# Kernel tuning notes

Hardware: AMD Instinct MI355X
Metric: run time of the kernel (lower is better)

## Reference

```python
import jax, jax.numpy as jnp
import numpy as np

HEADS = 4
DIM_HEAD = 32
CHUNK = 1024
GROUPS = 8
EPS = 1e-5


def setup_inputs() -> dict:
    key = jax.random.key(0)
    k1, k2, k3 = jax.random.split(key, 3)
    b, dim, h, w = 8, 64, 96, 96
    inner = HEADS * DIM_HEAD  # 128
    x = jax.random.normal(k1, (b, dim, h, w), dtype=jnp.float32)
    W_qkv = jax.random.normal(k2, (3 * inner, dim), dtype=jnp.float32) * (1.0 / np.sqrt(dim))
    W_out = jax.random.normal(k3, (dim, inner), dtype=jnp.float32) * (1.0 / np.sqrt(inner))
    b_out = jnp.zeros((dim,), dtype=jnp.float32)
    gamma = jnp.ones((dim,), dtype=jnp.float32)
    beta = jnp.zeros((dim,), dtype=jnp.float32)
    return {"x": x, "W_qkv": W_qkv, "W_out": W_out, "b_out": b_out,
            "gamma": gamma, "beta": beta}


def reference(x, W_qkv, W_out, b_out, gamma, beta):
    b, c, h, w = x.shape
    n = h * w
    nch = n // CHUNK  # number of full chunks (n chosen divisible by CHUNK)
    d = DIM_HEAD
    BH = b * HEADS

    # 1x1 conv (no bias) == matmul over channel dim
    xf = x.reshape(b, c, n)
    qkv = jnp.einsum('oc,bcn->bon', W_qkv, xf)          # [b, 3*inner, n]
    q, k, v = jnp.split(qkv, 3, axis=1)                  # each [b, inner, n]

    def chunkify(t):
        # [b, inner, n] -> [BH, nch, d, CHUNK]; slicing i:i+CHUNK on last axis
        # equals reshaping n -> (nch, CHUNK) in order.
        return t.reshape(BH, d, nch, CHUNK).transpose(0, 2, 1, 3)

    qc, kc, vc = chunkify(q), chunkify(k), chunkify(v)

    qs = jax.nn.softmax(qc, axis=-1)  # softmax over chunk spatial positions
    ks = jax.nn.softmax(kc, axis=-2)  # softmax over head channels

    # context = k_chunk^T @ v_chunk : [BH, nch, CHUNK, CHUNK]
    ctx = jnp.einsum('gkdi,gkdj->gkij', ks, vc)
    # chunk_out = q_chunk @ context : [BH, nch, d, CHUNK]
    out = jnp.einsum('gkdi,gkij->gkdj', qs, ctx)

    # concat chunks back along spatial dim, reshape to image layout
    out = out.transpose(0, 2, 1, 3).reshape(b, HEADS * d, h, w)

    # to_out: 1x1 conv with bias, then GroupNorm(8, dim)
    y = jnp.einsum('oc,bchw->bohw', W_out, out) + b_out[None, :, None, None]

    yg = y.reshape(b, GROUPS, c // GROUPS, h, w)
    mu = jnp.mean(yg, axis=(2, 3, 4), keepdims=True)
    var = jnp.var(yg, axis=(2, 3, 4), keepdims=True)
    yn = ((yg - mu) * jax.lax.rsqrt(var + EPS)).reshape(b, c, h, w)
    return yn * gamma[None, :, None, None] + beta[None, :, None, None]
```

## Files before the change

### kernel.cpp

```cpp
#include <hip/hip_runtime.h>
#include <hip/hip_bf16.h>

#define N_POS 9216
#define NCHUNK 9
#define BATCH 8
#define CDIM 64
#define HEADS 4
#define EPS 1e-5f

#define PPART_SZ ((size_t)32 * NCHUNK * 1024)
#define NPART 8
#define UBF_BYTES ((size_t)BATCH * NCHUNK * 64 * 128 * 2)

typedef __attribute__((ext_vector_type(8))) short short8;
typedef __attribute__((ext_vector_type(4))) float f32x4;

static __device__ inline unsigned pk2(float a, float b) {
    __hip_bfloat162 h2(__float2bfloat16(a), __float2bfloat16(b));
    return *reinterpret_cast<unsigned*>(&h2);
}
static __device__ inline float bf2f(short s) {
    union { unsigned u; float f; } c; c.u = ((unsigned)(unsigned short)s) << 16; return c.f;
}

__global__ __launch_bounds__(256) void wprep_kernel(const float* __restrict__ Wqkv,
        __hip_bfloat16* __restrict__ wbf, float* __restrict__ stats) {
    int i = blockIdx.x * 256 + threadIdx.x;
    if (i < 6144) {
        float4 v = ((const float4*)Wqkv)[i];
        uint2 u; u.x = pk2(v.x, v.y); u.y = pk2(v.z, v.w);
        ((uint2*)wbf)[i] = u;
    }
    if (i < 128) stats[i] = 0.f;
}

__global__ __launch_bounds__(256) void qkp_kernel(const float* __restrict__ x,
        const __hip_bfloat16* __restrict__ wbf, float* __restrict__ Pparts) {
    int bx = blockIdx.x;
    int b  = blockIdx.y;
    int ck = bx >> 3, pt = bx & 7;
    __shared__ __align__(16) char lraw[36864];
    __hip_bfloat16 (*xs)[72]  = (__hip_bfloat16(*)[72])lraw;
    __hip_bfloat16 (*skT)[72] = (__hip_bfloat16(*)[72])lraw;
    int t = threadIdx.x, w = t >> 6, l = t & 63;
    int l15 = l & 15, quad = l >> 4;

    f32x4 pac[2][2];
    pac[0][0] = (f32x4){0,0,0,0}; pac[0][1] = (f32x4){0,0,0,0};
    pac[1][0] = (f32x4){0,0,0,0}; pac[1][1] = (f32x4){0,0,0,0};

    for (int half = 0; half < 2; ++half) {
        int n0 = bx * 128 + half * 64;

        {
            int p = t & 63, cbase = (t >> 6) * 16;
            const float* xb = x + (size_t)b * CDIM * N_POS + n0 + p;
            #pragma unroll
            for (int j = 0; j < 16; j += 4) {
                float v0 = xb[(size_t)(cbase + j + 0) * N_POS];
                float v1 = xb[(size_t)(cbase + j + 1) * N_POS];
                float v2 = xb[(size_t)(cbase + j + 2) * N_POS];
                float v3 = xb[(size_t)(cbase + j + 3) * N_POS];
                uint2 u; u.x = pk2(v0, v1); u.y = pk2(v2, v3);
                *reinterpret_cast<uint2*>(&xs[p][cbase + j]) = u;
            }
        }
        __syncthreads();

        f32x4 acc[4][4];
        #pragma unroll
        for (int mt = 0; mt < 4; ++mt)
            #pragma unroll
            for (int nt = 0; nt < 4; ++nt) acc[mt][nt] = (f32x4){0.f, 0.f, 0.f, 0.f};
        #pragma unroll
        for (int ks = 0; ks < 2; ++ks) {
            int k0 = ks * 32 + quad * 8;
            short8 av[4];
            #pragma unroll
            for (int mt = 0; mt < 4; ++mt)
                av[mt] = *reinterpret_cast<const short8*>(&xs[mt * 16 + l15][k0]);
            #pragma unroll
            for (int nt = 0; nt < 4; ++nt) {
                short8 bw = *reinterpret_cast<const short8*>(wbf + (size_t)(w * 64 + nt * 16 + l15) * 64 + k0);
                #pragma unroll
                for (int mt = 0; mt < 4; ++mt)
                    acc[mt][nt] = __builtin_amdgcn_mfma_f32_16x16x32_bf16(av[mt], bw, acc[mt][nt], 0, 0, 0);
            }
        }
        __syncthreads();

        #pragma unroll
        for (int nt = 0; nt < 4; ++nt) {
            int ch = w * 64 + nt * 16 + l15;
            #pragma unroll
            for (int mt = 0; mt < 4; ++mt) {
                uint2 u;
                u.x = pk2(acc[mt][nt][0], acc[mt][nt][1]);
                u.y = pk2(acc[mt][nt][2], acc[mt][nt][3]);
                *reinterpret_cast<uint2*>(&skT[ch][mt * 16 + quad * 4]) = u;
            }
        }
        __syncthreads();

        {
            int p = t & 63, h = t >> 6;
            float kr[32]; float mx = -1e30f;
            #pragma unroll
            for (int d = 0; d < 32; ++d) { kr[d] = bf2f(*(const short*)&skT[128 + h * 32 + d][p]); mx = fmaxf(mx, kr[d]); }
            float s = 0.f;
            #pragma unroll
            for (int d = 0; d < 32; ++d) { kr[d] = __expf(kr[d] - mx); s += kr[d]; }
            float is = 1.f / s;
            #pragma unroll
            for (int d = 0; d < 32; ++d) skT[128 + h * 32 + d][p] = __float2bfloat16(kr[d] * is);
            #pragma unroll
            for (int d = 0; d < 32; ++d) {
                float qv = bf2f(*(const short*)&skT[h * 32 + d][p]);
                skT[h * 32 + d][p] = __float2bfloat16(__expf(qv));
            }
        }
        __syncthreads();

        #pragma unroll
        for (int step = 0; step < 2; ++step) {
            int k0 = step * 32 + quad * 8;
            short8 bk[2];
            #pragma unroll
            for (int nt = 0; nt < 2; ++nt)
                bk[nt] = *reinterpret_cast<const short8*>(&skT[128 + w * 32 + nt * 16 + l15][k0]);
            #pragma unroll
            for (int mt = 0; mt < 2; ++mt) {
                short8 aq = *reinterpret_cast<const short8*>(&skT[w * 32 + mt * 16 + l15][k0]);
                pac[mt][0] = __builtin_amdgcn_mfma_f32_16x16x32_bf16(aq, bk[0], pac[mt][0], 0, 0, 0);
                pac[mt][1] = __builtin_amdgcn_mfma_f32_16x16x32_bf16(aq, bk[1], pac[mt][1], 0, 0, 0);
            }
        }
        __syncthreads();
    }

    float* Pp = Pparts + (size_t)pt * PPART_SZ + ((size_t)(b * 4 + w) * NCHUNK + ck) * 1024;
    #pragma unroll
    for (int mt = 0; mt < 2; ++mt)
        #pragma unroll
        for (int nt = 0; nt < 2; ++nt)
            #pragma unroll
            for (int r = 0; r < 4; ++r)
                Pp[(mt * 16 + quad * 4 + r) * 32 + nt * 16 + l15] = pac[mt][nt][r];
}

__global__ __launch_bounds__(256) void umat_kernel(const float* __restrict__ Wout,
        const float* __restrict__ Pparts, __hip_bfloat16* __restrict__ Ubf) {
    int ck = blockIdx.x, b = blockIdx.y, h = blockIdx.z;
    int bh = b * 4 + h;
    int t = threadIdx.x;
    __shared__ float Pl[32][32];
    __shared__ float iZ[32];
    size_t base4 = ((size_t)bh * NCHUNK + ck) * 256;
    {
        const float4* P0 = (const float4*)Pparts + base4 + t;
        float4 s = (float4){0.f, 0.f, 0.f, 0.f};
        #pragma unroll
        for (int j = 0; j < NPART; ++j) {
            float4 a = P0[j * (PPART_SZ / 4)];
            s.x += a.x; s.y += a.y; s.z += a.z; s.w += a.w;
        }
        ((float4*)Pl)[t] = s;
    }
    __syncthreads();
    if (t < 32) {
        float s = 0.f;
        #pragma unroll
        for (int c = 0; c < 32; ++c) s += Pl[t][c];
        iZ[t] = 1.f / s;
    }
    __syncthreads();
    int o = t & 63, wv = t >> 6;
    float wz[32];
    {
        const float4* wr = (const float4*)(Wout + (size_t)o * 128 + h * 32);
        #pragma unroll
        for (int j = 0; j < 8; ++j) {
            float4 f = wr[j];
            wz[j*4+0] = f.x * iZ[j*4+0]; wz[j*4+1] = f.y * iZ[j*4+1];
            wz[j*4+2] = f.z * iZ[j*4+2]; wz[j*4+3] = f.w * iZ[j*4+3];
        }
    }
    float ua[8];
    #pragma unroll
    for (int j = 0; j < 8; ++j) ua[j] = 0.f;
    for (int d = 0; d < 32; ++d) {
        float wd = wz[d];
        #pragma unroll
        for (int j = 0; j < 8; ++j) ua[j] += wd * Pl[d][wv * 8 + j];
    }
    uint4 up;
    up.x = pk2(ua[0], ua[1]); up.y = pk2(ua[2], ua[3]);
    up.z = pk2(ua[4], ua[5]); up.w = pk2(ua[6], ua[7]);
    __hip_bfloat16* Up = Ubf + ((size_t)(b * NCHUNK + ck) * 64 + o) * 128 + h * 32 + wv * 8;
    *reinterpret_cast<uint4*>(Up) = up;
}

__global__ __launch_bounds__(256) void vy_kernel(const float* __restrict__ x,
        const __hip_bfloat16* __restrict__ wbf, const __hip_bfloat16* __restrict__ Ubf,
        const float* __restrict__ bout, float* __restrict__ y, float* __restrict__ stats) {
    int bx = blockIdx.x;
    int b  = blockIdx.y;
    int ck = bx >> 3;
    int n0 = bx * 128;
    __shared__ __align__(16) char lraw[34816];
    __hip_bfloat16 (*xs)[72]    = (__hip_bfloat16(*)[72])lraw;
    __hip_bfloat16 (*vbuf)[136] = (__hip_bfloat16(*)[136])lraw;
    __shared__ float gsum[8], gsq[8];
    int t = threadIdx.x, w = t >> 6, l = t & 63;
    int l15 = l & 15, quad = l >> 4;
    if (t < 8) { gsum[t] = 0.f; gsq[t] = 0.f; }

    {
        int p = t & 127, cbase = (t >> 7) * 32;
        const float* xb = x + (size_t)b * CDIM * N_POS + n0 + p;
        #pragma unroll
        for (int j = 0; j < 32; j += 4) {
            float v0 = xb[(size_t)(cbase + j + 0) * N_POS];
            float v1 = xb[(size_t)(cbase + j + 1) * N_POS];
            float v2 = xb[(size_t)(cbase + j + 2) * N_POS];
            float v3 = xb[(size_t)(cbase + j + 3) * N_POS];
            uint2 u; u.x = pk2(v0, v1); u.y = pk2(v2, v3);
            *reinterpret_cast<uint2*>(&xs[p][cbase + j]) = u;
        }
    }
    __syncthreads();

    int nw = w * 32;
    {
        f32x4 vacc[8][2];
        #pragma unroll
        for (int mt = 0; mt < 8; ++mt) { vacc[mt][0] = (f32x4){0,0,0,0}; vacc[mt][1] = (f32x4){0,0,0,0}; }
        #pragma unroll
        for (int ks = 0; ks < 2; ++ks) {
            int k0 = ks * 32 + quad * 8;
            short8 bfr[2];
            #pragma unroll
            for (int nt = 0; nt < 2; ++nt)
                bfr[nt] = *reinterpret_cast<const short8*>(&xs[nw + nt * 16 + l15][k0]);
            #pragma unroll
            for (int mt = 0; mt < 8; ++mt) {
                short8 afr = *reinterpret_cast<const short8*>(wbf + (size_t)(256 + mt * 16 + l15) * 64 + k0);
                vacc[mt][0] = __builtin_amdgcn_mfma_f32_16x16x32_bf16(afr, bfr[0], vacc[mt][0], 0, 0, 0);
                vacc[mt][1] = __builtin_amdgcn_mfma_f32_16x16x32_bf16(afr, bfr[1], vacc[mt][1], 0, 0, 0);
            }
        }
        __syncthreads();

        #pragma unroll
        for (int mt = 0; mt < 8; ++mt)
            #pragma unroll
            for (int nt = 0; nt < 2; ++nt) {
                int p = nw + nt * 16 + l15;
                uint2 u;
                u.x = pk2(vacc[mt][nt][0], vacc[mt][nt][1]);
                u.y = pk2(vacc[mt][nt][2], vacc[mt][nt][3]);
                *reinterpret_cast<uint2*>(&vbuf[p][mt * 16 + quad * 4]) = u;
            }
    }
    __syncthreads();

    const __hip_bfloat16* Ub = Ubf + (size_t)(b * NCHUNK + ck) * 64 * 128;
    f32x4 acc[4][2];
    #pragma unroll
    for (int mt = 0; mt < 4; ++mt) { acc[mt][0] = (f32x4){0,0,0,0}; acc[mt][1] = (f32x4){0,0,0,0}; }
    #pragma unroll
    for (int ks = 0; ks < 4; ++ks) {
        int k0 = ks * 32 + quad * 8;
        short8 bf[2];
        #pragma unroll
        for (int nt = 0; nt < 2; ++nt)
            bf[nt] = *reinterpret_cast<const short8*>(&vbuf[nw + nt * 16 + l15][k0]);
        #pragma unroll
        for (int mt = 0; mt < 4; ++mt) {
            short8 af = *reinterpret_cast<const short8*>(Ub + (size_t)(mt * 16 + l15) * 128 + k0);
            acc[mt][0] = __builtin_amdgcn_mfma_f32_16x16x32_bf16(af, bf[0], acc[mt][0], 0, 0, 0);
            acc[mt][1] = __builtin_amdgcn_mfma_f32_16x16x32_bf16(af, bf[1], acc[mt][1], 0, 0, 0);
        }
    }
    float gsl[4], gql[4];
    #pragma unroll
    for (int mt = 0; mt < 4; ++mt) { gsl[mt] = 0.f; gql[mt] = 0.f; }
    float* yb = y + (size_t)b * CDIM * N_POS;
    int nbase = n0 + nw;
    #pragma unroll
    for (int mt = 0; mt < 4; ++mt) {
        float4 bo = *reinterpret_cast<const float4*>(bout + mt * 16 + quad * 4);
        const float* bop = reinterpret_cast<const float*>(&bo);
        #pragma unroll
        for (int nt = 0; nt < 2; ++nt) {
            int n = nbase + nt * 16 + l15;
            #pragma unroll
            for (int r = 0; r < 4; ++r) {
                int o = mt * 16 + quad * 4 + r;
                float val = acc[mt][nt][r] + bop[r];
                yb[(size_t)o * N_POS + n] = val;
                gsl[mt] += val; gql[mt] += val * val;
            }
        }
    }
    #pragma unroll
    for (int off = 16; off >= 1; off >>= 1) {
        #pragma unroll
        for (int mt = 0; mt < 4; ++mt) {
            gsl[mt] += __shfl_xor(gsl[mt], off, 64);
            gql[mt] += __shfl_xor(gql[mt], off, 64);
        }
    }
    if (l == 0 || l == 32) {
        int qh = quad >> 1;
        #pragma unroll
        for (int mt = 0; mt < 4; ++mt) {
            atomicAdd(&gsum[2 * mt + qh], gsl[mt]);
            atomicAdd(&gsq[2 * mt + qh], gql[mt]);
        }
    }
    __syncthreads();
    if (t < 8) {
        atomicAdd(&stats[(b * 8 + t) * 2],     gsum[t]);
        atomicAdd(&stats[(b * 8 + t) * 2 + 1], gsq[t]);
    }
}

__global__ __launch_bounds__(256) void gn_kernel(float* __restrict__ y,
        const float* __restrict__ stats, const float* __restrict__ gamma,
        const float* __restrict__ beta) {
    int i4 = blockIdx.x * 256 + threadIdx.x;
    if (i4 >= (BATCH * CDIM * N_POS) / 4) return;
    int base = i4 * 4;
    int bc = base / N_POS;
    int c = bc & 63, b = bc >> 6;
    int g = c >> 3;
    float s = stats[(b * 8 + g) * 2], q = stats[(b * 8 + g) * 2 + 1];
    const float invN = 1.f / (8.f * N_POS);
    float mean = s * invN;
    float var = q * invN - mean * mean;
    float sc = rsqrtf(var + EPS);
    float ga = gamma[c] * sc;
    float be = beta[c] - mean * sc * gamma[c];
    float4 v = ((float4*)y)[i4];
    v.x = v.x * ga + be; v.y = v.y * ga + be; v.z = v.z * ga + be; v.w = v.w * ga + be;
    ((float4*)y)[i4] = v;
}

extern "C" void kernel_launch(void* const* d_in, const int* in_sizes, int n_in,
                              void* d_out, int out_size, void* d_ws, size_t ws_size,
                              hipStream_t stream) {
    const float* x     = (const float*)d_in[0];
    const float* Wqkv  = (const float*)d_in[1];
    const float* Wout  = (const float*)d_in[2];
    const float* bout  = (const float*)d_in[3];
    const float* gamma = (const float*)d_in[4];
    const float* beta  = (const float*)d_in[5];
    float* out = (float*)d_out;

    float* stats  = (float*)d_ws;
    float* Pparts = stats + 128;
    __hip_bfloat16* Ubf = (__hip_bfloat16*)(Pparts + NPART * PPART_SZ);
    __hip_bfloat16* wbf = (__hip_bfloat16*)((char*)Ubf + UBF_BYTES);

    wprep_kernel<<<dim3(24), 256, 0, stream>>>(Wqkv, wbf, stats);
    qkp_kernel<<<dim3(72, BATCH), 256, 0, stream>>>(x, wbf, Pparts);
    umat_kernel<<<dim3(NCHUNK, BATCH, HEADS), 256, 0, stream>>>(Wout, Pparts, Ubf);
    vy_kernel<<<dim3(72, BATCH), 256, 0, stream>>>(x, wbf, Ubf, bout, out, stats);
    gn_kernel<<<dim3((BATCH * CDIM * N_POS / 4 + 255) / 256), 256, 0, stream>>>(out, stats, gamma, beta);
}
```

Measured before the change: 125.5 us.

## Fuse GroupNorm into vy kernel via grid-wide barrier, keep y in registers

Removes the separate GroupNorm pass by keeping the to_out accumulators in registers. Every block waits at a global atomic-counter barrier until all 576 blocks have contributed group statistics, then normalizes and writes y once. This avoids writing y, reading it back and rewriting it, roughly 19 MB each way. It relies on all 576 blocks being co-resident (launch bounds of 3 blocks per CU); if they are not, the kernel deadlocks. The barrier also puts a global sync inside the kernel.

```diff
diff --git a/kernel.cpp b/kernel.cpp
--- a/kernel.cpp
+++ b/kernel.cpp
@@ -11,6 +11,7 @@
 #define PPART_SZ ((size_t)32 * NCHUNK * 1024)
 #define NPART 8
 #define UBF_BYTES ((size_t)BATCH * NCHUNK * 64 * 128 * 2)
+#define VY_BLOCKS 576u
 
 typedef __attribute__((ext_vector_type(8))) short short8;
 typedef __attribute__((ext_vector_type(4))) float f32x4;
@@ -31,7 +32,7 @@
         uint2 u; u.x = pk2(v.x, v.y); u.y = pk2(v.z, v.w);
         ((uint2*)wbf)[i] = u;
     }
-    if (i < 128) stats[i] = 0.f;
+    if (i < 256) stats[i] = 0.f;
 }
 
 __global__ __launch_bounds__(256) void qkp_kernel(const float* __restrict__ x,
@@ -51,7 +52,6 @@
 
     for (int half = 0; half < 2; ++half) {
         int n0 = bx * 128 + half * 64;
-
         {
             int p = t & 63, cbase = (t >> 6) * 16;
             const float* xb = x + (size_t)b * CDIM * N_POS + n0 + p;
@@ -200,9 +200,10 @@
     *reinterpret_cast<uint4*>(Up) = up;
 }
 
-__global__ __launch_bounds__(256) void vy_kernel(const float* __restrict__ x,
+__global__ __launch_bounds__(256, 3) void vy_kernel(const float* __restrict__ x,
         const __hip_bfloat16* __restrict__ wbf, const __hip_bfloat16* __restrict__ Ubf,
-        const float* __restrict__ bout, float* __restrict__ y, float* __restrict__ stats) {
+        const float* __restrict__ bout, float* __restrict__ y, float* __restrict__ stats,
+        const float* __restrict__ gamma, const float* __restrict__ beta) {
     int bx = blockIdx.x;
     int b  = blockIdx.y;
     int ck = bx >> 3;
@@ -250,7 +251,6 @@
             }
         }
         __syncthreads();
-
         #pragma unroll
         for (int mt = 0; mt < 8; ++mt)
             #pragma unroll
@@ -285,23 +285,18 @@
     float gsl[4], gql[4];
     #pragma unroll
     for (int mt = 0; mt < 4; ++mt) { gsl[mt] = 0.f; gql[mt] = 0.f; }
-    float* yb = y + (size_t)b * CDIM * N_POS;
-    int nbase = n0 + nw;
     #pragma unroll
     for (int mt = 0; mt < 4; ++mt) {
         float4 bo = *reinterpret_cast<const float4*>(bout + mt * 16 + quad * 4);
         const float* bop = reinterpret_cast<const float*>(&bo);
         #pragma unroll
-        for (int nt = 0; nt < 2; ++nt) {
-            int n = nbase + nt * 16 + l15;
+        for (int nt = 0; nt < 2; ++nt)
             #pragma unroll
             for (int r = 0; r < 4; ++r) {
-                int o = mt * 16 + quad * 4 + r;
                 float val = acc[mt][nt][r] + bop[r];
-                yb[(size_t)o * N_POS + n] = val;
+                acc[mt][nt][r] = val;
                 gsl[mt] += val; gql[mt] += val * val;
             }
-        }
     }
     #pragma unroll
     for (int off = 16; off >= 1; off >>= 1) {
@@ -324,27 +319,43 @@
         atomicAdd(&stats[(b * 8 + t) * 2],     gsum[t]);
         atomicAdd(&stats[(b * 8 + t) * 2 + 1], gsq[t]);
     }
-}
-
-__global__ __launch_bounds__(256) void gn_kernel(float* __restrict__ y,
-        const float* __restrict__ stats, const float* __restrict__ gamma,
-        const float* __restrict__ beta) {
-    int i4 = blockIdx.x * 256 + threadIdx.x;
-    if (i4 >= (BATCH * CDIM * N_POS) / 4) return;
-    int base = i4 * 4;
-    int bc = base / N_POS;
-    int c = bc & 63, b = bc >> 6;
-    int g = c >> 3;
-    float s = stats[(b * 8 + g) * 2], q = stats[(b * 8 + g) * 2 + 1];
+    __threadfence();
+    __syncthreads();
+    if (t == 0) {
+        unsigned* ctr = (unsigned*)(stats + 192);
+        __hip_atomic_fetch_add(ctr, 1u, __ATOMIC_RELEASE, __HIP_MEMORY_SCOPE_AGENT);
+        while (__hip_atomic_load(ctr, __ATOMIC_ACQUIRE, __HIP_MEMORY_SCOPE_AGENT) < VY_BLOCKS)
+            __builtin_amdgcn_s_sleep(8);
+    }
+    __syncthreads();
+
     const float invN = 1.f / (8.f * N_POS);
-    float mean = s * invN;
-    float var = q * invN - mean * mean;
-    float sc = rsqrtf(var + EPS);
-    float ga = gamma[c] * sc;
-    float be = beta[c] - mean * sc * gamma[c];
-    float4 v = ((float4*)y)[i4];
-    v.x = v.x * ga + be; v.y = v.y * ga + be; v.z = v.z * ga + be; v.w = v.w * ga + be;
-    ((float4*)y)[i4] = v;
+    float* yb = y + (size_t)b * CDIM * N_POS;
+    int nbase = n0 + nw;
+    #pragma unroll
+    for (int mt = 0; mt < 4; ++mt) {
+        int g = 2 * mt + (quad >> 1);
+        float s = __hip_atomic_load(&stats[(b * 8 + g) * 2],     __ATOMIC_RELAXED, __HIP_MEMORY_SCOPE_AGENT);
+        float q = __hip_atomic_load(&stats[(b * 8 + g) * 2 + 1], __ATOMIC_RELAXED, __HIP_MEMORY_SCOPE_AGENT);
+        float mean = s * invN;
+        float var = q * invN - mean * mean;
+        float rstd = rsqrtf(var + EPS);
+        float4 ga4 = *reinterpret_cast<const float4*>(gamma + mt * 16 + quad * 4);
+        float4 be4 = *reinterpret_cast<const float4*>(beta + mt * 16 + quad * 4);
+        const float* gap = reinterpret_cast<const float*>(&ga4);
+        const float* bep = reinterpret_cast<const float*>(&be4);
+        #pragma unroll
+        for (int r = 0; r < 4; ++r) {
+            int o = mt * 16 + quad * 4 + r;
+            float sc = gap[r] * rstd;
+            float be = bep[r] - mean * sc;
+            #pragma unroll
+            for (int nt = 0; nt < 2; ++nt) {
+                int n = nbase + nt * 16 + l15;
+                yb[(size_t)o * N_POS + n] = acc[mt][nt][r] * sc + be;
+            }
+        }
+    }
 }
 
 extern "C" void kernel_launch(void* const* d_in, const int* in_sizes, int n_in,
@@ -359,13 +370,12 @@
     float* out = (float*)d_out;
 
     float* stats  = (float*)d_ws;
-    float* Pparts = stats + 128;
+    float* Pparts = stats + 256;
     __hip_bfloat16* Ubf = (__hip_bfloat16*)(Pparts + NPART * PPART_SZ);
     __hip_bfloat16* wbf = (__hip_bfloat16*)((char*)Ubf + UBF_BYTES);
 
     wprep_kernel<<<dim3(24), 256, 0, stream>>>(Wqkv, wbf, stats);
     qkp_kernel<<<dim3(72, BATCH), 256, 0, stream>>>(x, wbf, Pparts);
     umat_kernel<<<dim3(NCHUNK, BATCH, HEADS), 256, 0, stream>>>(Wout, Pparts, Ubf);
-    vy_kernel<<<dim3(72, BATCH), 256, 0, stream>>>(x, wbf, Ubf, bout, out, stats);
-    gn_kernel<<<dim3((BATCH * CDIM * N_POS / 4 + 255) / 256), 256, 0, stream>>>(out, stats, gamma, beta);
-}
+    vy_kernel<<<dim3(72, BATCH), 256, 0, stream>>>(x, wbf, Ubf, bout, out, stats, gamma, beta);
+}
```

New measurement: 198.5 us. 1.58x slower.
